# Kernel optimization log

Measured on AMD Instinct MI355X. Metric: run time of the kernel, lower is better.

Reference implementation:

```python
import jax, jax.numpy as jnp
import numpy as np
import math

B, H, S, D = 2, 16, 2048, 64

def setup_inputs() -> dict:
    key = jax.random.key(0)
    kq, kk, kv = jax.random.split(key, 3)
    Q = jax.random.normal(kq, (B, H, S, D), dtype=jnp.float32)
    K = jax.random.normal(kk, (B, H, S, D), dtype=jnp.float32)
    V = jax.random.normal(kv, (B, H, S, D), dtype=jnp.float32)
    causal_mask = jnp.tril(jnp.ones((S, S), dtype=bool))
    return {"Q": Q, "K": K, "V": V, "causal_mask": causal_mask}

def reference(Q, K, V, causal_mask):
    d_k = K.shape[-1]
    scores = jnp.einsum('bhqd,bhkd->bhqk', Q, K) / math.sqrt(d_k)
    scores = jnp.where(causal_mask, scores, -jnp.inf)
    probs = jax.nn.softmax(scores, axis=-1)
    return jnp.einsum('bhqk,bhkd->bhqd', probs, V)
```

## Files before the change

### kernel.cpp

```cpp
#include <hip/hip_runtime.h>
#include <math.h>


constexpr int kS   = 2048;
constexpr int kD   = 64;
constexpr int kBH  = 32;
constexpr int kPadP = 72;

typedef short short8 __attribute__((ext_vector_type(8)));
typedef float float4v __attribute__((ext_vector_type(4)));
typedef float float16v __attribute__((ext_vector_type(16)));
typedef unsigned int u32;
typedef unsigned short u16;

static __device__ inline u16 f2bf(float f) {
  union { float f; unsigned u; } v; v.f = f;
  unsigned r = v.u + 0x7FFF + ((v.u >> 16) & 1);
  return (u16)(r >> 16);
}

static __device__ inline short8 pack8(float4v a, float4v b) {
  short8 r;
  r[0] = (short)f2bf(a[0]); r[1] = (short)f2bf(a[1]);
  r[2] = (short)f2bf(a[2]); r[3] = (short)f2bf(a[3]);
  r[4] = (short)f2bf(b[0]); r[5] = (short)f2bf(b[1]);
  r[6] = (short)f2bf(b[2]); r[7] = (short)f2bf(b[3]);
  return r;
}

static __device__ inline void swap32(u32 a, u32 b, u32& oa, u32& ob) {
#if __has_builtin(__builtin_amdgcn_permlane32_swap)
  auto r = __builtin_amdgcn_permlane32_swap(a, b, false, false);
  oa = r[0]; ob = r[1];
#else
  asm volatile("v_permlane32_swap_b32 %0, %1" : "+v"(a), "+v"(b));
  oa = a; ob = b;
#endif
}

__global__ __launch_bounds__(256)
void prep_kernel(const float* __restrict__ Q, const float* __restrict__ K,
                 const float* __restrict__ V,
                 u16* __restrict__ Qb, u16* __restrict__ Kb, u16* __restrict__ VT) {
  __shared__ u16 tile[64 * kPadP];
  const int tid = threadIdx.x;
  const int bh = blockIdx.y, st = blockIdx.x;
  const size_t ibase = (size_t)bh * kS * kD + (size_t)st * 64 * kD;
  const int r  = tid >> 2;
  const int c0 = (tid & 3) * 16;
  {
    const float scl = 0.125f * 1.44269504089f;
    const float* qp = Q + ibase + (size_t)r * kD + c0;
    float4v a = *(const float4v*)(qp);
    float4v b = *(const float4v*)(qp + 4);
    float4v c = *(const float4v*)(qp + 8);
    float4v d = *(const float4v*)(qp + 12);
    #pragma unroll
    for (int i = 0; i < 4; ++i) { a[i] *= scl; b[i] *= scl; c[i] *= scl; d[i] *= scl; }
    u16* dst = Qb + ibase + (size_t)r * kD + c0;
    *(short8*)dst       = pack8(a, b);
    *(short8*)(dst + 8) = pack8(c, d);
  }
  {
    const float* kp = K + ibase + (size_t)r * kD + c0;
    float4v a = *(const float4v*)(kp);
    float4v b = *(const float4v*)(kp + 4);
    float4v c = *(const float4v*)(kp + 8);
    float4v d = *(const float4v*)(kp + 12);
    u16* dst = Kb + ibase + (size_t)r * kD + c0;
    *(short8*)dst       = pack8(a, b);
    *(short8*)(dst + 8) = pack8(c, d);
  }
  {
    const float* vp = V + ibase + (size_t)r * kD + c0;
    float4v a = *(const float4v*)(vp);
    float4v b = *(const float4v*)(vp + 4);
    float4v c = *(const float4v*)(vp + 8);
    float4v d = *(const float4v*)(vp + 12);
    u16* t = &tile[r * kPadP + c0];
    *(short8*)t       = pack8(a, b);
    *(short8*)(t + 8) = pack8(c, d);
  }
  __syncthreads();
  {
    const int dd = tid >> 2;
    const int s0 = (tid & 3) * 16;
    short8 w0, w1;
    #pragma unroll
    for (int i = 0; i < 8; ++i) {
      w0[i] = (short)tile[(s0 + i) * kPadP + dd];
      w1[i] = (short)tile[(s0 + 8 + i) * kPadP + dd];
    }
    u16* vdst = VT + (size_t)bh * kD * kS + (size_t)dd * kS + st * 64 + s0;
    *(short8*)vdst       = w0;
    *(short8*)(vdst + 8) = w1;
  }
}

__global__ __launch_bounds__(256, 2)
void fattn_kernel(const u16* __restrict__ Qb, const u16* __restrict__ Kb,
                  const u16* __restrict__ VT, float* __restrict__ O) {
  const int tid  = threadIdx.x;
  const int wave = tid >> 6;
  const int lane = tid & 63;
  const int l31  = lane & 31;
  const int h    = lane >> 5;

  const int bh = blockIdx.y;
  const int j  = blockIdx.x;

  const int we = ((bh + j) & 1) ? (3 - wave) : wave;
  const int s  = (we & 2) ? ((we & 1) ? 63 - j : 32 + j)
                          : ((we & 1) ? 31 - j : j);
  const int q0 = s * 32;

  const size_t base  = (size_t)bh * kS * kD;
  const size_t vbase = (size_t)bh * kD * kS;

  float16v zf;
  #pragma unroll
  for (int i = 0; i < 16; ++i) zf[i] = 0.f;

  short8 ones;
  #pragma unroll
  for (int i = 0; i < 8; ++i) ones[i] = (short)0x3F80;

  short8 qf[4];
  {
    const u16* qp = Qb + base + (size_t)(q0 + l31) * kD + h * 8;
    #pragma unroll
    for (int dk = 0; dk < 4; ++dk) qf[dk] = *(const short8*)(qp + dk * 16);
  }

  const u16* kptr = Kb + base + (size_t)l31 * kD + h * 8;
  const u16* vp0  = VT + vbase + (size_t)l31 * kS + h * 8;
  const u16* vp1  = vp0 + (size_t)32 * kS;

  float16v acc0 = zf, acc1 = zf, lacc = zf;

  short8 kfA[4], kfB[4];
  #pragma unroll
  for (int dk = 0; dk < 4; ++dk) kfA[dk] = *(const short8*)(kptr + dk * 16);

  const int qg = q0 + l31;

  auto step = [&](short8* kfc, short8* kfn, int k) {
    const u16* vk0 = vp0 + k * 32;
    const u16* vk1 = vp1 + k * 32;
    const short8 vf0 = *(const short8*)(vk0);
    const short8 vf1 = *(const short8*)(vk1);
    const short8 vf2 = *(const short8*)(vk0 + 16);
    const short8 vf3 = *(const short8*)(vk1 + 16);
    {
      const int kn = (k < s) ? (k + 1) : k;
      const u16* kp = kptr + (size_t)kn * 2048;
      #pragma unroll
      for (int dk = 0; dk < 4; ++dk) kfn[dk] = *(const short8*)(kp + dk * 16);
    }

    __builtin_amdgcn_s_setprio(1);
    float16v sv = __builtin_amdgcn_mfma_f32_32x32x16_bf16(kfc[0], qf[0], zf, 0, 0, 0);
    sv = __builtin_amdgcn_mfma_f32_32x32x16_bf16(kfc[1], qf[1], sv, 0, 0, 0);
    sv = __builtin_amdgcn_mfma_f32_32x32x16_bf16(kfc[2], qf[2], sv, 0, 0, 0);
    sv = __builtin_amdgcn_mfma_f32_32x32x16_bf16(kfc[3], qf[3], sv, 0, 0, 0);
    __builtin_amdgcn_s_setprio(0);

    if (k == s) {
      #pragma unroll
      for (int r = 0; r < 16; ++r) {
        const int kg = k * 32 + (r & 3) + 8 * (r >> 2) + 4 * h;
        if (kg > qg) sv[r] = -1e30f;
      }
    }

    u32 pk[8];
    #pragma unroll
    for (int g2 = 0; g2 < 4; ++g2) {
      const u32 u0 = __float_as_uint(__builtin_amdgcn_exp2f(sv[4 * g2 + 0]));
      const u32 u1 = __float_as_uint(__builtin_amdgcn_exp2f(sv[4 * g2 + 1]));
      const u32 u2 = __float_as_uint(__builtin_amdgcn_exp2f(sv[4 * g2 + 2]));
      const u32 u3 = __float_as_uint(__builtin_amdgcn_exp2f(sv[4 * g2 + 3]));
      pk[2 * g2]     = __builtin_amdgcn_perm(u1, u0, 0x07060302u);
      pk[2 * g2 + 1] = __builtin_amdgcn_perm(u3, u2, 0x07060302u);
    }

    {
      union { u32 u[4]; short8 s8; } pf;
      swap32(pk[0], pk[2], pf.u[0], pf.u[2]);
      swap32(pk[1], pk[3], pf.u[1], pf.u[3]);
      __builtin_amdgcn_s_setprio(1);
      acc0 = __builtin_amdgcn_mfma_f32_32x32x16_bf16(pf.s8, vf0, acc0, 0, 0, 0);
      acc1 = __builtin_amdgcn_mfma_f32_32x32x16_bf16(pf.s8, vf1, acc1, 0, 0, 0);
      lacc = __builtin_amdgcn_mfma_f32_32x32x16_bf16(pf.s8, ones, lacc, 0, 0, 0);
      __builtin_amdgcn_s_setprio(0);
    }
    {
      union { u32 u[4]; short8 s8; } pf;
      swap32(pk[4], pk[6], pf.u[0], pf.u[2]);
      swap32(pk[5], pk[7], pf.u[1], pf.u[3]);
      __builtin_amdgcn_s_setprio(1);
      acc0 = __builtin_amdgcn_mfma_f32_32x32x16_bf16(pf.s8, vf2, acc0, 0, 0, 0);
      acc1 = __builtin_amdgcn_mfma_f32_32x32x16_bf16(pf.s8, vf3, acc1, 0, 0, 0);
      lacc = __builtin_amdgcn_mfma_f32_32x32x16_bf16(pf.s8, ones, lacc, 0, 0, 0);
      __builtin_amdgcn_s_setprio(0);
    }
  };

  int k = 0;
  while (true) {
    step(kfA, kfB, k); if (++k > s) break;
    step(kfB, kfA, k); if (++k > s) break;
  }

  #pragma unroll
  for (int r = 0; r < 16; ++r) {
    const int row = (r & 3) + 8 * (r >> 2) + 4 * h;
    const float inv = 1.f / lacc[r];
    float* op = O + ((size_t)bh * kS + q0 + row) * kD;
    op[l31]      = acc0[r] * inv;
    op[l31 + 32] = acc1[r] * inv;
  }
}

extern "C" void kernel_launch(void* const* d_in, const int* in_sizes, int n_in,
                              void* d_out, int out_size, void* d_ws, size_t ws_size,
                              hipStream_t stream) {
  const float* Q = (const float*)d_in[0];
  const float* K = (const float*)d_in[1];
  const float* V = (const float*)d_in[2];
  float* O = (float*)d_out;

  const size_t nKV = (size_t)kBH * kS * kD;
  u16* Qb = (u16*)d_ws;
  u16* Kb = Qb + nKV;
  u16* VT = Kb + nKV;

  dim3 gprep(kS / 64, kBH);
  prep_kernel<<<gprep, 256, 0, stream>>>(Q, K, V, Qb, Kb, VT);
  dim3 grid(16, kBH);
  fattn_kernel<<<grid, 256, 0, stream>>>(Qb, Kb, VT, O);
}
```

Measured before the change: 165.9 us.

## Store Q/K/V in MFMA fragment order and launch one-wave blocks longest-first

The prep kernel now writes Q, K and V in a per-32-row fragment layout, so each lane's short8 operand is contiguous and a wave load covers a full 1KB chunk instead of strided rows. The attention kernel becomes a single-wave block, with 2048 blocks ordered so the longest causal rows launch first and adjacent heads interleave, replacing the 4-wave blocks with paired scheduling. V fragments are now double-buffered together with K. Single-wave blocks lose any sharing within a block and depend on the hardware block scheduler for load balance.

```diff
diff --git a/kernel.cpp b/kernel.cpp
--- a/kernel.cpp
+++ b/kernel.cpp
@@ -6,6 +6,7 @@
 constexpr int kD   = 64;
 constexpr int kBH  = 32;
 constexpr int kPadP = 72;
+constexpr int kFragBH = 64 * 4 * 512;
 
 typedef short short8 __attribute__((ext_vector_type(8)));
 typedef float float4v __attribute__((ext_vector_type(4)));
@@ -41,13 +42,17 @@
 __global__ __launch_bounds__(256)
 void prep_kernel(const float* __restrict__ Q, const float* __restrict__ K,
                  const float* __restrict__ V,
-                 u16* __restrict__ Qb, u16* __restrict__ Kb, u16* __restrict__ VT) {
+                 u16* __restrict__ Qf, u16* __restrict__ Kf, u16* __restrict__ Vf) {
   __shared__ u16 tile[64 * kPadP];
   const int tid = threadIdx.x;
   const int bh = blockIdx.y, st = blockIdx.x;
   const size_t ibase = (size_t)bh * kS * kD + (size_t)st * 64 * kD;
+  const size_t fbase = (size_t)bh * kFragBH;
   const int r  = tid >> 2;
   const int c0 = (tid & 3) * 16;
+  const int dk = tid & 3;
+  const int U  = st * 2 + (r >> 5);
+  const int lr = r & 31;
   {
     const float scl = 0.125f * 1.44269504089f;
     const float* qp = Q + ibase + (size_t)r * kD + c0;
@@ -57,9 +62,9 @@
     float4v d = *(const float4v*)(qp + 12);
     #pragma unroll
     for (int i = 0; i < 4; ++i) { a[i] *= scl; b[i] *= scl; c[i] *= scl; d[i] *= scl; }
-    u16* dst = Qb + ibase + (size_t)r * kD + c0;
-    *(short8*)dst       = pack8(a, b);
-    *(short8*)(dst + 8) = pack8(c, d);
+    u16* dst = Qf + fbase + (size_t)(U * 4 + dk) * 512;
+    *(short8*)(dst + lr * 8)        = pack8(a, b);
+    *(short8*)(dst + (32 + lr) * 8) = pack8(c, d);
   }
   {
     const float* kp = K + ibase + (size_t)r * kD + c0;
@@ -67,9 +72,9 @@
     float4v b = *(const float4v*)(kp + 4);
     float4v c = *(const float4v*)(kp + 8);
     float4v d = *(const float4v*)(kp + 12);
-    u16* dst = Kb + ibase + (size_t)r * kD + c0;
-    *(short8*)dst       = pack8(a, b);
-    *(short8*)(dst + 8) = pack8(c, d);
+    u16* dst = Kf + fbase + (size_t)(U * 4 + dk) * 512;
+    *(short8*)(dst + lr * 8)        = pack8(a, b);
+    *(short8*)(dst + (32 + lr) * 8) = pack8(c, d);
   }
   {
     const float* vp = V + ibase + (size_t)r * kD + c0;
@@ -91,31 +96,32 @@
       w0[i] = (short)tile[(s0 + i) * kPadP + dd];
       w1[i] = (short)tile[(s0 + 8 + i) * kPadP + dd];
     }
-    u16* vdst = VT + (size_t)bh * kD * kS + (size_t)dd * kS + st * 64 + s0;
-    *(short8*)vdst       = w0;
-    *(short8*)(vdst + 8) = w1;
-  }
-}
-
-__global__ __launch_bounds__(256, 2)
-void fattn_kernel(const u16* __restrict__ Qb, const u16* __restrict__ Kb,
-                  const u16* __restrict__ VT, float* __restrict__ O) {
-  const int tid  = threadIdx.x;
-  const int wave = tid >> 6;
-  const int lane = tid & 63;
+    const int ku   = st * 2 + (s0 >> 5);
+    const int koff = s0 & 31;
+    const int c    = ((koff >> 4) << 1) | (dd >> 5);
+    u16* vdst = Vf + fbase + (size_t)(ku * 4 + c) * 512;
+    *(short8*)(vdst + (dd & 31) * 8)        = w0;
+    *(short8*)(vdst + (32 + (dd & 31)) * 8) = w1;
+  }
+}
+
+__global__ __launch_bounds__(64, 2)
+void fattn_kernel(const u16* __restrict__ Qf, const u16* __restrict__ Kf,
+                  const u16* __restrict__ Vf, float* __restrict__ O) {
+  const int lane = threadIdx.x;
   const int l31  = lane & 31;
   const int h    = lane >> 5;
 
-  const int bh = blockIdx.y;
-  const int j  = blockIdx.x;
-
-  const int we = ((bh + j) & 1) ? (3 - wave) : wave;
-  const int s  = (we & 2) ? ((we & 1) ? 63 - j : 32 + j)
-                          : ((we & 1) ? 31 - j : j);
-  const int q0 = s * 32;
-
-  const size_t base  = (size_t)bh * kS * kD;
-  const size_t vbase = (size_t)bh * kD * kS;
+  const int orig = ((blockIdx.x & 7) << 8) | (blockIdx.x >> 3);
+  const int pr   = orig >> 7;
+  const int r2   = orig & 127;
+  const int s    = 63 - (r2 >> 1);
+  const int bh   = pr * 2 + (r2 & 1);
+  const int q0   = s * 32;
+
+  const size_t fb = (size_t)bh * kFragBH;
+  const u16* kp = Kf + fb + lane * 8;
+  const u16* vp = Vf + fb + lane * 8;
 
   float16v zf;
   #pragma unroll
@@ -127,42 +133,32 @@
 
   short8 qf[4];
   {
-    const u16* qp = Qb + base + (size_t)(q0 + l31) * kD + h * 8;
-    #pragma unroll
-    for (int dk = 0; dk < 4; ++dk) qf[dk] = *(const short8*)(qp + dk * 16);
-  }
-
-  const u16* kptr = Kb + base + (size_t)l31 * kD + h * 8;
-  const u16* vp0  = VT + vbase + (size_t)l31 * kS + h * 8;
-  const u16* vp1  = vp0 + (size_t)32 * kS;
+    const u16* qp = Qf + fb + (size_t)(s * 4) * 512 + lane * 8;
+    #pragma unroll
+    for (int dk = 0; dk < 4; ++dk) qf[dk] = *(const short8*)(qp + dk * 512);
+  }
 
   float16v acc0 = zf, acc1 = zf, lacc = zf;
-
-  short8 kfA[4], kfB[4];
-  #pragma unroll
-  for (int dk = 0; dk < 4; ++dk) kfA[dk] = *(const short8*)(kptr + dk * 16);
-
   const int qg = q0 + l31;
 
-  auto step = [&](short8* kfc, short8* kfn, int k) {
-    const u16* vk0 = vp0 + k * 32;
-    const u16* vk1 = vp1 + k * 32;
-    const short8 vf0 = *(const short8*)(vk0);
-    const short8 vf1 = *(const short8*)(vk1);
-    const short8 vf2 = *(const short8*)(vk0 + 16);
-    const short8 vf3 = *(const short8*)(vk1 + 16);
-    {
-      const int kn = (k < s) ? (k + 1) : k;
-      const u16* kp = kptr + (size_t)kn * 2048;
-      #pragma unroll
-      for (int dk = 0; dk < 4; ++dk) kfn[dk] = *(const short8*)(kp + dk * 16);
-    }
+  short8 kA[4], vA[4], kB[4], vB[4];
+  #pragma unroll
+  for (int dk = 0; dk < 4; ++dk) kA[dk] = *(const short8*)(kp + dk * 512);
+  #pragma unroll
+  for (int c = 0; c < 4; ++c)    vA[c]  = *(const short8*)(vp + c * 512);
+
+  auto step = [&](const short8* kc, const short8* vc, short8* kn, short8* vn, int k) {
+    const int knext = (k < s) ? (k + 1) : k;
+    #pragma unroll
+    for (int dk = 0; dk < 4; ++dk) kn[dk] = *(const short8*)(kp + knext * 2048 + dk * 512);
+    #pragma unroll
+    for (int c = 0; c < 4; ++c)    vn[c]  = *(const short8*)(vp + knext * 2048 + c * 512);
 
     __builtin_amdgcn_s_setprio(1);
-    float16v sv = __builtin_amdgcn_mfma_f32_32x32x16_bf16(kfc[0], qf[0], zf, 0, 0, 0);
-    sv = __builtin_amdgcn_mfma_f32_32x32x16_bf16(kfc[1], qf[1], sv, 0, 0, 0);
-    sv = __builtin_amdgcn_mfma_f32_32x32x16_bf16(kfc[2], qf[2], sv, 0, 0, 0);
-    sv = __builtin_amdgcn_mfma_f32_32x32x16_bf16(kfc[3], qf[3], sv, 0, 0, 0);
+    float16v sv = __builtin_amdgcn_mfma_f32_32x32x16_bf16(kc[0], qf[0], zf, 0, 0, 0);
+    sv = __builtin_amdgcn_mfma_f32_32x32x16_bf16(kc[1], qf[1], sv, 0, 0, 0);
+    sv = __builtin_amdgcn_mfma_f32_32x32x16_bf16(kc[2], qf[2], sv, 0, 0, 0);
+    sv = __builtin_amdgcn_mfma_f32_32x32x16_bf16(kc[3], qf[3], sv, 0, 0, 0);
     __builtin_amdgcn_s_setprio(0);
 
     if (k == s) {
@@ -189,9 +185,9 @@
       swap32(pk[0], pk[2], pf.u[0], pf.u[2]);
       swap32(pk[1], pk[3], pf.u[1], pf.u[3]);
       __builtin_amdgcn_s_setprio(1);
-      acc0 = __builtin_amdgcn_mfma_f32_32x32x16_bf16(pf.s8, vf0, acc0, 0, 0, 0);
-      acc1 = __builtin_amdgcn_mfma_f32_32x32x16_bf16(pf.s8, vf1, acc1, 0, 0, 0);
-      lacc = __builtin_amdgcn_mfma_f32_32x32x16_bf16(pf.s8, ones, lacc, 0, 0, 0);
+      acc0 = __builtin_amdgcn_mfma_f32_32x32x16_bf16(pf.s8, vc[0], acc0, 0, 0, 0);
+      acc1 = __builtin_amdgcn_mfma_f32_32x32x16_bf16(pf.s8, vc[1], acc1, 0, 0, 0);
+      lacc = __builtin_amdgcn_mfma_f32_32x32x16_bf16(pf.s8, ones,  lacc, 0, 0, 0);
       __builtin_amdgcn_s_setprio(0);
     }
     {
@@ -199,17 +195,17 @@
       swap32(pk[4], pk[6], pf.u[0], pf.u[2]);
       swap32(pk[5], pk[7], pf.u[1], pf.u[3]);
       __builtin_amdgcn_s_setprio(1);
-      acc0 = __builtin_amdgcn_mfma_f32_32x32x16_bf16(pf.s8, vf2, acc0, 0, 0, 0);
-      acc1 = __builtin_amdgcn_mfma_f32_32x32x16_bf16(pf.s8, vf3, acc1, 0, 0, 0);
-      lacc = __builtin_amdgcn_mfma_f32_32x32x16_bf16(pf.s8, ones, lacc, 0, 0, 0);
+      acc0 = __builtin_amdgcn_mfma_f32_32x32x16_bf16(pf.s8, vc[2], acc0, 0, 0, 0);
+      acc1 = __builtin_amdgcn_mfma_f32_32x32x16_bf16(pf.s8, vc[3], acc1, 0, 0, 0);
+      lacc = __builtin_amdgcn_mfma_f32_32x32x16_bf16(pf.s8, ones,  lacc, 0, 0, 0);
       __builtin_amdgcn_s_setprio(0);
     }
   };
 
   int k = 0;
   while (true) {
-    step(kfA, kfB, k); if (++k > s) break;
-    step(kfB, kfA, k); if (++k > s) break;
+    step(kA, vA, kB, vB, k); if (++k > s) break;
+    step(kB, vB, kA, vA, k); if (++k > s) break;
   }
 
   #pragma unroll
@@ -231,12 +227,11 @@
   float* O = (float*)d_out;
 
   const size_t nKV = (size_t)kBH * kS * kD;
-  u16* Qb = (u16*)d_ws;
-  u16* Kb = Qb + nKV;
-  u16* VT = Kb + nKV;
+  u16* Qf = (u16*)d_ws;
+  u16* Kf = Qf + nKV;
+  u16* Vf = Kf + nKV;
 
   dim3 gprep(kS / 64, kBH);
-  prep_kernel<<<gprep, 256, 0, stream>>>(Q, K, V, Qb, Kb, VT);
-  dim3 grid(16, kBH);
-  fattn_kernel<<<grid, 256, 0, stream>>>(Qb, Kb, VT, O);
-}
+  prep_kernel<<<gprep, 256, 0, stream>>>(Q, K, V, Qf, Kf, Vf);
+  fattn_kernel<<<2048, 64, 0, stream>>>(Qf, Kf, Vf, O);
+}
```

New measurement: 142.9 us. 13.8% less time.
